# Kernel tuning notes

Hardware: AMD Instinct MI355X
Metric: run time of the kernel (lower is better)

The kernel has to match this reference:

```python
import jax, jax.numpy as jnp
import numpy as np

K = 2.0          # arctan surrogate sharpness (init kwarg k)
THRESHOLD = 1.0  # init kwarg threshold


def _binop(ei, ej):
    # linear recurrence combine: (A, Bu) pairs, v_t = A_t*v_{t-1} + Bu_t
    a_i, b_i = ei
    a_j, b_j = ej
    return a_j * a_i, a_j * b_i + b_j


def _pscan(tau, x):
    # x: [B, T, H]; tau: [H] broadcast over batch and time (matches
    # jnp.repeat(tau[None], T, 0) inside vmap over batch in the original).
    tau_b = jnp.broadcast_to(tau, x.shape)
    _, v = jax.lax.associative_scan(_binop, (tau_b, x), axis=1)
    return v


@jax.custom_vjp
def _spike(x):
    # spyx arctan surrogate: forward is Heaviside, backward 1/(1+(k*x)^2)
    return jnp.where(x > 0, 1.0, 0.0).astype(x.dtype)


def _spike_fwd(x):
    return _spike(x), x


def _spike_bwd(x, g):
    return (g / (1.0 + (K * x) ** 2),)


_spike.defvjp(_spike_fwd, _spike_bwd)


def setup_inputs() -> dict:
    key = jax.random.key(0)
    k1, k2 = jax.random.split(key)
    x = jax.random.normal(k1, (16, 1024, 1024), dtype=jnp.float32)
    # beta ~ TruncatedNormal(mean=0.25, std=0.5), as in hk.initializers
    beta = 0.25 + 0.5 * jax.random.truncated_normal(k2, -2.0, 2.0, (1024,), jnp.float32)
    return {"x": x, "beta": beta}


def reference(x, beta):
    b = jnp.clip(beta, 0.0, 1.0)
    V = _pscan(b, x)                      # membrane potential scan
    R = _pscan(b, jax.nn.sigmoid(V))      # refractory/reset scan
    return _spike(V - R - THRESHOLD), V
```

## Files before the change

kernel.cpp:

```cpp
#include <hip/hip_runtime.h>


#define BB 16
#define TT 1024
#define HH 1024
#define L 8
#define C 128
#define G 8

typedef float f4 __attribute__((ext_vector_type(4)));

__device__ __forceinline__ f4 fma4(f4 a, f4 b, f4 c) {
    f4 r;
#pragma unroll
    for (int k = 0; k < 4; ++k) r[k] = fmaf(a[k], b[k], c[k]);
    return r;
}

__global__ __launch_bounds__(1024, 8) void lif_scan(const float* __restrict__ x,
                                                    const float* __restrict__ beta,
                                                    float* __restrict__ out_spike,
                                                    float* __restrict__ out_v) {
    __shared__ f4 lds_v[C][G];
    __shared__ f4 lds_r[C][G];

    const int tid = threadIdx.x;
    const int g = tid & (G - 1);
    const int c = tid >> 3;
    const int blk = blockIdx.x;
    const int b = blk >> 5;
    const int h0 = ((blk & 31) << 5) + (g << 2);

    f4 bf = *reinterpret_cast<const f4*>(beta + h0);
#pragma unroll
    for (int k = 0; k < 4; ++k) bf[k] = fminf(fmaxf(bf[k], 0.0f), 1.0f);
    f4 pw = bf;
#pragma unroll
    for (int k = 0; k < 3; ++k) pw *= pw;

    const size_t base = (size_t)b * TT * HH + (size_t)(c * L) * HH + (size_t)h0;
    const f4* __restrict__ xv = reinterpret_cast<const f4*>(x + base);
    f4* __restrict__ vv = reinterpret_cast<f4*>(out_v + base);
    f4* __restrict__ sv = reinterpret_cast<f4*>(out_spike + base);
    const int STRD = HH / 4;

    f4 V = (f4)0.0f;
#pragma unroll
    for (int i = 0; i < L; ++i) V = fma4(bf, V, xv[(size_t)i * STRD]);
    lds_v[c][g] = V;
    __syncthreads();

    f4 Vstart = (f4)0.0f;
    for (int j = 0; j < c; ++j) Vstart = fma4(pw, Vstart, lds_v[j][g]);

    V = Vstart;
    f4 R = (f4)0.0f;
#pragma unroll
    for (int i = 0; i < L; ++i) {
        V = fma4(bf, V, xv[(size_t)i * STRD]);
        vv[(size_t)i * STRD] = V;
        f4 sg;
#pragma unroll
        for (int k = 0; k < 4; ++k) sg[k] = __builtin_amdgcn_rcpf(1.0f + __expf(-V[k]));
        R = fma4(bf, R, sg);
    }
    lds_r[c][g] = R;
    __syncthreads();

    f4 Rstart = (f4)0.0f;
    for (int j = 0; j < c; ++j) Rstart = fma4(pw, Rstart, lds_r[j][g]);

    R = Rstart;
#pragma unroll
    for (int i = 0; i < L; ++i) {
        const f4 vf = vv[(size_t)i * STRD];
        f4 sg;
#pragma unroll
        for (int k = 0; k < 4; ++k) sg[k] = __builtin_amdgcn_rcpf(1.0f + __expf(-vf[k]));
        R = fma4(bf, R, sg);
        f4 sp;
#pragma unroll
        for (int k = 0; k < 4; ++k) sp[k] = (vf[k] - R[k] > 1.0f) ? 1.0f : 0.0f;
        __builtin_nontemporal_store(sp, sv + (size_t)i * STRD);
    }
}

extern "C" void kernel_launch(void* const* d_in, const int* in_sizes, int n_in,
                              void* d_out, int out_size, void* d_ws, size_t ws_size,
                              hipStream_t stream) {
    const float* x = (const float*)d_in[0];
    const float* beta = (const float*)d_in[1];
    float* out = (float*)d_out;
    float* out_spike = out;
    float* out_v = out + (size_t)BB * TT * HH;

    const int grid = (BB * HH) / 32;
    lif_scan<<<grid, 1024, 0, stream>>>(x, beta, out_spike, out_v);
}
```

Baseline: 199.5 us.

## Split fused LIF scan into three kernels with global chunk carries

Replaces the single block-local scan, where each 1024-thread block covered all of T for 32 channels and passed carries through LDS, with three kernels. The first computes per-chunk V sums, the second applies the V carry and writes V along with per-chunk R sums, and the third applies the R carry and writes spikes. Carries now go through a global workspace instead of LDS with syncthreads. The aim is to remove the serial in-block carry loops and barriers and to use wider blocks covering all H per batch and time chunk. In exchange, x is read twice, V is written and read back, and there are extra launches and workspace traffic.

```diff
diff --git a/kernel.cpp b/kernel.cpp
--- a/kernel.cpp
+++ b/kernel.cpp
@@ -4,9 +4,9 @@
 #define BB 16
 #define TT 1024
 #define HH 1024
-#define L 8
-#define C 128
-#define G 8
+#define TC 32
+#define NC 32
+#define STRD4 (HH / 4)
 
 typedef float f4 __attribute__((ext_vector_type(4)));
 
@@ -17,63 +17,87 @@
     return r;
 }
 
-__global__ __launch_bounds__(1024, 8) void lif_scan(const float* __restrict__ x,
-                                                    const float* __restrict__ beta,
-                                                    float* __restrict__ out_spike,
-                                                    float* __restrict__ out_v) {
-    __shared__ f4 lds_v[C][G];
-    __shared__ f4 lds_r[C][G];
-
-    const int tid = threadIdx.x;
-    const int g = tid & (G - 1);
-    const int c = tid >> 3;
-    const int blk = blockIdx.x;
-    const int b = blk >> 5;
-    const int h0 = ((blk & 31) << 5) + (g << 2);
-
+__device__ __forceinline__ f4 load_beta(const float* beta, int h0) {
     f4 bf = *reinterpret_cast<const f4*>(beta + h0);
 #pragma unroll
     for (int k = 0; k < 4; ++k) bf[k] = fminf(fmaxf(bf[k], 0.0f), 1.0f);
-    f4 pw = bf;
+    return bf;
+}
+
+__global__ __launch_bounds__(256) void k_vsum(const float* __restrict__ x,
+                                              const float* __restrict__ beta,
+                                              float* __restrict__ S) {
+    const int blk = blockIdx.x;
+    const int b = blk >> 5, tc = blk & 31;
+    const int h0 = threadIdx.x << 2;
+    const f4 bf = load_beta(beta, h0);
+
+    const f4* __restrict__ xv =
+        reinterpret_cast<const f4*>(x + ((size_t)b * TT + (size_t)tc * TC) * HH + h0);
+    f4 V = (f4)0.0f;
 #pragma unroll
-    for (int k = 0; k < 3; ++k) pw *= pw;
+    for (int t = 0; t < TC; ++t) V = fma4(bf, V, xv[(size_t)t * STRD4]);
+    *reinterpret_cast<f4*>(S + ((size_t)b * NC + tc) * HH + h0) = V;
+}
 
-    const size_t base = (size_t)b * TT * HH + (size_t)(c * L) * HH + (size_t)h0;
+__global__ __launch_bounds__(256) void k_vpass(const float* __restrict__ x,
+                                               const float* __restrict__ beta,
+                                               const float* __restrict__ S,
+                                               float* __restrict__ Rsum,
+                                               float* __restrict__ out_v) {
+    const int blk = blockIdx.x;
+    const int b = blk >> 5, tc = blk & 31;
+    const int h0 = threadIdx.x << 2;
+    const f4 bf = load_beta(beta, h0);
+    f4 A = bf;
+#pragma unroll
+    for (int k = 0; k < 5; ++k) A *= A;
+
+    f4 Vs = (f4)0.0f;
+    for (int j = 0; j < tc; ++j)
+        Vs = fma4(A, Vs, *reinterpret_cast<const f4*>(S + ((size_t)b * NC + j) * HH + h0));
+
+    const size_t base = ((size_t)b * TT + (size_t)tc * TC) * HH + h0;
     const f4* __restrict__ xv = reinterpret_cast<const f4*>(x + base);
     f4* __restrict__ vv = reinterpret_cast<f4*>(out_v + base);
-    f4* __restrict__ sv = reinterpret_cast<f4*>(out_spike + base);
-    const int STRD = HH / 4;
 
-    f4 V = (f4)0.0f;
+    f4 V = Vs, R = (f4)0.0f;
 #pragma unroll
-    for (int i = 0; i < L; ++i) V = fma4(bf, V, xv[(size_t)i * STRD]);
-    lds_v[c][g] = V;
-    __syncthreads();
-
-    f4 Vstart = (f4)0.0f;
-    for (int j = 0; j < c; ++j) Vstart = fma4(pw, Vstart, lds_v[j][g]);
-
-    V = Vstart;
-    f4 R = (f4)0.0f;
-#pragma unroll
-    for (int i = 0; i < L; ++i) {
-        V = fma4(bf, V, xv[(size_t)i * STRD]);
-        vv[(size_t)i * STRD] = V;
+    for (int t = 0; t < TC; ++t) {
+        V = fma4(bf, V, xv[(size_t)t * STRD4]);
+        vv[(size_t)t * STRD4] = V;
         f4 sg;
 #pragma unroll
         for (int k = 0; k < 4; ++k) sg[k] = __builtin_amdgcn_rcpf(1.0f + __expf(-V[k]));
         R = fma4(bf, R, sg);
     }
-    lds_r[c][g] = R;
-    __syncthreads();
+    *reinterpret_cast<f4*>(Rsum + ((size_t)b * NC + tc) * HH + h0) = R;
+}
 
-    f4 Rstart = (f4)0.0f;
-    for (int j = 0; j < c; ++j) Rstart = fma4(pw, Rstart, lds_r[j][g]);
+__global__ __launch_bounds__(256) void k_spike(const float* __restrict__ beta,
+                                               const float* __restrict__ Rsum,
+                                               const float* __restrict__ out_v,
+                                               float* __restrict__ out_s) {
+    const int blk = blockIdx.x;
+    const int b = blk >> 5, tc = blk & 31;
+    const int h0 = threadIdx.x << 2;
+    const f4 bf = load_beta(beta, h0);
+    f4 A = bf;
+#pragma unroll
+    for (int k = 0; k < 5; ++k) A *= A;
 
-    R = Rstart;
+    f4 Rs = (f4)0.0f;
+    for (int j = 0; j < tc; ++j)
+        Rs = fma4(A, Rs, *reinterpret_cast<const f4*>(Rsum + ((size_t)b * NC + j) * HH + h0));
+
+    const size_t base = ((size_t)b * TT + (size_t)tc * TC) * HH + h0;
+    const f4* __restrict__ vv = reinterpret_cast<const f4*>(out_v + base);
+    f4* __restrict__ sv = reinterpret_cast<f4*>(out_s + base);
+
+    f4 R = Rs;
 #pragma unroll
-    for (int i = 0; i < L; ++i) {
-        const f4 vf = vv[(size_t)i * STRD];
+    for (int t = 0; t < TC; ++t) {
+        const f4 vf = vv[(size_t)t * STRD4];
         f4 sg;
 #pragma unroll
         for (int k = 0; k < 4; ++k) sg[k] = __builtin_amdgcn_rcpf(1.0f + __expf(-vf[k]));
@@ -81,7 +105,7 @@
         f4 sp;
 #pragma unroll
         for (int k = 0; k < 4; ++k) sp[k] = (vf[k] - R[k] > 1.0f) ? 1.0f : 0.0f;
-        __builtin_nontemporal_store(sp, sv + (size_t)i * STRD);
+        __builtin_nontemporal_store(sp, sv + (size_t)t * STRD4);
     }
 }
 
@@ -93,7 +117,11 @@
     float* out = (float*)d_out;
     float* out_spike = out;
     float* out_v = out + (size_t)BB * TT * HH;
+    float* S = (float*)d_ws;
+    float* Rsum = S + (size_t)BB * NC * HH;
 
-    const int grid = (BB * HH) / 32;
-    lif_scan<<<grid, 1024, 0, stream>>>(x, beta, out_spike, out_v);
+    const int grid = BB * NC;
+    k_vsum<<<grid, 256, 0, stream>>>(x, beta, S);
+    k_vpass<<<grid, 256, 0, stream>>>(x, beta, S, Rsum, out_v);
+    k_spike<<<grid, 256, 0, stream>>>(beta, Rsum, out_v, out_spike);
 }
```

New measurement: 205.6 us. +3.1%, slower.
